# Performance work log

Measured on AMD Instinct MI355X. Metric: run time of the kernel, lower is better.

The kernel has to match this reference:

```python
import jax, jax.numpy as jnp
import numpy as np
import math

B, NH, SQ, HD = 4, 32, 512, 128
MLEN = 3584


def setup_inputs() -> dict:
    key = jax.random.key(0)
    k1, k2, k3, k4 = jax.random.split(key, 4)
    q = jax.random.normal(k1, (B, NH, SQ, HD), dtype=jnp.float32)
    k = jax.random.normal(k2, (B, NH, SQ, HD), dtype=jnp.float32)
    v = jax.random.normal(k3, (B, NH, SQ, HD), dtype=jnp.float32)
    mem = jax.random.normal(k4, (B, MLEN, 2 * NH * HD), dtype=jnp.float32)
    mask = jnp.ones((B, 1, SQ, MLEN + SQ), dtype=jnp.float32)
    return {"q": q, "k": k, "v": v, "mask": mask, "mem": mem}


def reference(q, k, v, mask, mem):
    b, nh, sq, hd = k.shape
    mlen = mem.shape[1]
    # cache_kv: stack (k,v) -> (2,b,nh,sq,hd), permute -> (b,sq,2,nh,hd), flatten
    cache_kv = jnp.stack((k, v)).transpose(1, 3, 0, 2, 4).reshape(b, sq, 2 * nh * hd)
    # split cached mem into memk/memv: (b,mlen,2,nh,hd) -> (2,b,nh,mlen,hd)
    mem_r = mem.reshape(b, mlen, 2, nh, hd).transpose(2, 0, 3, 1, 4)
    k_full = jnp.concatenate([mem_r[0], k], axis=2)  # [b,nh,mlen+sq,hd]
    v_full = jnp.concatenate([mem_r[1], v], axis=2)
    scale = 1.0 / math.sqrt(hd)
    scores = jnp.einsum("bhqd,bhkd->bhqk", q * scale, k_full)
    # standard_attention general mask path (mask.shape[-2] != 1)
    scores = scores * mask - 10000.0 * (1.0 - mask)
    probs = jax.nn.softmax(scores, axis=-1)
    context = jnp.einsum("bhqk,bhkd->bhqd", probs, v_full)
    return context, cache_kv
```

## Files before the change

kernel.cpp:

```cpp
#include <hip/hip_runtime.h>

#define B_ 4
#define NH_ 32
#define SQ_ 512
#define HD_ 128
#define MLEN_ 3584
#define KT_ 4096
#define QB_ 128
#define KB_ 64
#define NTILE_ 64
#define MEMTILES_ 56

typedef float f32x4 __attribute__((ext_vector_type(4)));
typedef short s16x8 __attribute__((ext_vector_type(8)));

__device__ __forceinline__ f32x4 MFMA16(s16x8 a, s16x8 b, f32x4 c) {
    return __builtin_amdgcn_mfma_f32_16x16x32_bf16(a, b, c, 0, 0, 0);
}

__device__ __forceinline__ s16x8 cvt8(float4 a, float4 b) {
    union { s16x8 v; __bf16 h[8]; } u;
    u.h[0] = (__bf16)a.x; u.h[1] = (__bf16)a.y;
    u.h[2] = (__bf16)a.z; u.h[3] = (__bf16)a.w;
    u.h[4] = (__bf16)b.x; u.h[5] = (__bf16)b.y;
    u.h[6] = (__bf16)b.z; u.h[7] = (__bf16)b.w;
    return u.v;
}

__launch_bounds__(512, 4)
__global__ void attn_kernel(const float* __restrict__ q, const float* __restrict__ k,
                            const float* __restrict__ v, const float* __restrict__ mask,
                            const float* __restrict__ mem, float* __restrict__ ctx)
{
    __shared__ __bf16 Klds[KB_ * HD_];
    __shared__ __bf16 Vt[HD_ * KB_];
    __shared__ __bf16 Plds[8 * 16 * KB_];

    const int tid  = threadIdx.x;
    const int lane = tid & 63;
    const int w    = tid >> 6;
    const int l15  = lane & 15;
    const int l4   = lane >> 4;
    const int xv   = (lane & 7) << 4;

    const int qt   = blockIdx.x >> 7;
    const int pair = blockIdx.x & 127;
    const int b    = pair >> 5;
    const int h    = pair & 31;
    const int q0   = qt * QB_;

    const float scale = 0.088388347648318447f;
    s16x8 qf[4];
    {
        const float* qbase = q + (((size_t)(b * NH_ + h)) * SQ_ + q0 + w * 16 + l15) * HD_;
        #pragma unroll
        for (int kc = 0; kc < 4; ++kc) {
            const float* p = qbase + kc * 32 + l4 * 8;
            float4 a = *(const float4*)p;
            float4 c = *(const float4*)(p + 4);
            a.x *= scale; a.y *= scale; a.z *= scale; a.w *= scale;
            c.x *= scale; c.y *= scale; c.z *= scale; c.w *= scale;
            qf[kc] = cvt8(a, c);
        }
    }

    f32x4 acc[8];
    #pragma unroll
    for (int n = 0; n < 8; ++n) acc[n] = (f32x4){0.f, 0.f, 0.f, 0.f};

    float mrun[4], lrun[4];
    #pragma unroll
    for (int i = 0; i < 4; ++i) { mrun[i] = -3.0e38f; lrun[i] = 0.f; }

    const float* maskbase = mask + ((size_t)b * SQ_ + q0 + w * 16 + l4 * 4) * KT_;

    for (int t = 0; t < NTILE_; ++t) {
        const int kv0 = t * KB_;
        const float *srcK, *srcV;
        int rstride;
        if (t < MEMTILES_) {
            const float* mrow = mem + ((size_t)b * MLEN_ + kv0) * (2 * NH_ * HD_) + h * HD_;
            srcK = mrow;
            srcV = mrow + NH_ * HD_;
            rstride = 2 * NH_ * HD_;
        } else {
            size_t off = (((size_t)b * NH_ + h) * SQ_ + (kv0 - MLEN_)) * HD_;
            srcK = k + off;
            srcV = v + off;
            rstride = HD_;
        }

        __syncthreads();

        #pragma unroll
        for (int it = 0; it < 2; ++it) {
            int idx = tid + it * 512;
            int row = idx >> 4, cg = idx & 15;
            const float* p = srcK + (size_t)row * rstride + cg * 8;
            float4 a = *(const float4*)p;
            float4 c = *(const float4*)(p + 4);
            s16x8 vv = cvt8(a, c);
            int byte = row * 256 + ((cg * 16) ^ ((row & 7) << 4));
            *(s16x8*)((char*)Klds + byte) = vv;
        }
        #pragma unroll
        for (int it = 0; it < 2; ++it) {
            int idx = tid + it * 512;
            int hd = idx & 127, kvb = idx >> 7;
            const float* p = srcV + (size_t)(kvb * 8) * rstride + hd;
            union { s16x8 v; __bf16 hh[8]; } u;
            #pragma unroll
            for (int j = 0; j < 8; ++j) u.hh[j] = (__bf16)p[(size_t)j * rstride];
            int byte = hd * 128 + ((kvb * 16) ^ ((hd & 7) << 4));
            *(s16x8*)((char*)Vt + byte) = u.v;
        }

        float mpre[4][4];
        #pragma unroll
        for (int i = 0; i < 4; ++i) {
            const float* mp = maskbase + (size_t)i * KT_ + kv0 + l15;
            #pragma unroll
            for (int n = 0; n < 4; ++n) mpre[i][n] = mp[n * 16];
        }

        __syncthreads();

        f32x4 sa[4];
        #pragma unroll
        for (int n = 0; n < 4; ++n) sa[n] = (f32x4){0.f, 0.f, 0.f, 0.f};
        #pragma unroll
        for (int n = 0; n < 4; ++n) {
            #pragma unroll
            for (int kc = 0; kc < 4; ++kc) {
                s16x8 kf = *(const s16x8*)((const char*)Klds +
                            (n * 16 + l15) * 256 + (((kc * 4 + l4) * 16) ^ xv));
                sa[n] = MFMA16(qf[kc], kf, sa[n]);
            }
        }

        #pragma unroll
        for (int i = 0; i < 4; ++i) {
            sa[0][i] = fmaf(mpre[i][0], sa[0][i] + 10000.f, -10000.f);
            sa[1][i] = fmaf(mpre[i][1], sa[1][i] + 10000.f, -10000.f);
            sa[2][i] = fmaf(mpre[i][2], sa[2][i] + 10000.f, -10000.f);
            sa[3][i] = fmaf(mpre[i][3], sa[3][i] + 10000.f, -10000.f);

            float rm = fmaxf(fmaxf(sa[0][i], sa[1][i]), fmaxf(sa[2][i], sa[3][i]));
            rm = fmaxf(rm, __shfl_xor(rm, 1));
            rm = fmaxf(rm, __shfl_xor(rm, 2));
            rm = fmaxf(rm, __shfl_xor(rm, 4));
            rm = fmaxf(rm, __shfl_xor(rm, 8));

            float om = mrun[i];
            float nm = fmaxf(om, rm);
            float al = __expf(om - nm);
            mrun[i] = nm;

            float rs = 0.f;
            #pragma unroll
            for (int n = 0; n < 4; ++n) {
                float pe = __expf(sa[n][i] - nm);
                sa[n][i] = pe;
                rs += pe;
            }
            rs += __shfl_xor(rs, 1);
            rs += __shfl_xor(rs, 2);
            rs += __shfl_xor(rs, 4);
            rs += __shfl_xor(rs, 8);
            lrun[i] = lrun[i] * al + rs;

            #pragma unroll
            for (int nn = 0; nn < 8; ++nn) acc[nn][i] *= al;
        }

        __bf16* pw = &Plds[w * (16 * KB_)];
        #pragma unroll
        for (int n = 0; n < 4; ++n)
            #pragma unroll
            for (int i = 0; i < 4; ++i) {
                int row = l4 * 4 + i;
                int col = n * 16 + l15;
                int byte = row * 128 + ((col * 2) ^ ((row & 7) << 4));
                *(__bf16*)((char*)pw + byte) = (__bf16)sa[n][i];
            }

        s16x8 pf[2];
        #pragma unroll
        for (int kt = 0; kt < 2; ++kt)
            pf[kt] = *(const s16x8*)((const char*)pw +
                          l15 * 128 + ((kt * 64 + l4 * 16) ^ xv));
        #pragma unroll
        for (int nn = 0; nn < 8; ++nn) {
            s16x8 vf0 = *(const s16x8*)((const char*)Vt +
                          (nn * 16 + l15) * 128 + ((l4 * 16) ^ xv));
            s16x8 vf1 = *(const s16x8*)((const char*)Vt +
                          (nn * 16 + l15) * 128 + ((64 + l4 * 16) ^ xv));
            acc[nn] = MFMA16(pf[0], vf0, acc[nn]);
            acc[nn] = MFMA16(pf[1], vf1, acc[nn]);
        }
    }

    float* obase = ctx + (((size_t)(b * NH_ + h)) * SQ_ + q0 + w * 16 + l4 * 4) * HD_ + l15;
    #pragma unroll
    for (int i = 0; i < 4; ++i) {
        float inv = 1.f / lrun[i];
        #pragma unroll
        for (int nn = 0; nn < 8; ++nn)
            obase[(size_t)i * HD_ + nn * 16] = acc[nn][i] * inv;
    }
}

__global__ void cachekv_kernel(const float* __restrict__ k, const float* __restrict__ v,
                               float* __restrict__ out)
{
    size_t i = ((size_t)blockIdx.x * 256 + threadIdx.x) * 4;
    unsigned f = (unsigned)i;
    unsigned d    = f & 127;
    unsigned hh   = (f >> 7) & 31;
    unsigned part = (f >> 12) & 1;
    unsigned s    = (f >> 13) & 511;
    unsigned bb   = f >> 22;
    const float* src = (part ? v : k) + (((size_t)(bb * 32u + hh)) * 512u + s) * 128u + d;
    *(float4*)(out + i) = *(const float4*)src;
}

extern "C" void kernel_launch(void* const* d_in, const int* in_sizes, int n_in,
                              void* d_out, int out_size, void* d_ws, size_t ws_size,
                              hipStream_t stream) {
    const float* q    = (const float*)d_in[0];
    const float* k    = (const float*)d_in[1];
    const float* v    = (const float*)d_in[2];
    const float* mask = (const float*)d_in[3];
    const float* mem  = (const float*)d_in[4];
    float* out = (float*)d_out;

    attn_kernel<<<dim3(B_ * NH_ * (SQ_ / QB_)), dim3(512), 0, stream>>>(q, k, v, mask, mem, out);

    const int ctx_elems = B_ * NH_ * SQ_ * HD_;
    const int ckv_elems = B_ * SQ_ * 2 * NH_ * HD_;
    cachekv_kernel<<<dim3(ckv_elems / 4 / 256), dim3(256), 0, stream>>>(k, v, out + ctx_elems);
    (void)in_sizes; (void)n_in; (void)out_size; (void)d_ws; (void)ws_size;
}
```

Before: 346.3 us.

## Compute transposed scores so P stays in registers, skip rescale when max stable

Swaps the MFMA operand order so each lane holds the scores for a single query row. The row max and row sum then need only two cross-lane shuffles, and the mask is read with vector loads. The shared-memory round trip for P is replaced by register shuffles that rebuild the bf16 A-operand layout. A lazy rescale skips the accumulator rescaling when the new row max stays within a threshold of the running max. This trades LDS traffic for extra shuffle instructions and a data-dependent branch.

```diff
diff --git a/kernel.cpp b/kernel.cpp
--- a/kernel.cpp
+++ b/kernel.cpp
@@ -34,7 +34,6 @@
 {
     __shared__ __bf16 Klds[KB_ * HD_];
     __shared__ __bf16 Vt[HD_ * KB_];
-    __shared__ __bf16 Plds[8 * 16 * KB_];
 
     const int tid  = threadIdx.x;
     const int lane = tid & 63;
@@ -68,11 +67,9 @@
     #pragma unroll
     for (int n = 0; n < 8; ++n) acc[n] = (f32x4){0.f, 0.f, 0.f, 0.f};
 
-    float mrun[4], lrun[4];
-    #pragma unroll
-    for (int i = 0; i < 4; ++i) { mrun[i] = -3.0e38f; lrun[i] = 0.f; }
-
-    const float* maskbase = mask + ((size_t)b * SQ_ + q0 + w * 16 + l4 * 4) * KT_;
+    float mrun = -3.0e38f, lrun = 0.f;
+
+    const float* maskrow = mask + ((size_t)b * SQ_ + q0 + w * 16 + l15) * KT_;
 
     for (int t = 0; t < NTILE_; ++t) {
         const int kv0 = t * KB_;
@@ -115,98 +112,125 @@
             *(s16x8*)((char*)Vt + byte) = u.v;
         }
 
-        float mpre[4][4];
-        #pragma unroll
-        for (int i = 0; i < 4; ++i) {
-            const float* mp = maskbase + (size_t)i * KT_ + kv0 + l15;
-            #pragma unroll
-            for (int n = 0; n < 4; ++n) mpre[i][n] = mp[n * 16];
-        }
-
         __syncthreads();
 
-        f32x4 sa[4];
-        #pragma unroll
-        for (int n = 0; n < 4; ++n) sa[n] = (f32x4){0.f, 0.f, 0.f, 0.f};
-        #pragma unroll
-        for (int n = 0; n < 4; ++n) {
+        f32x4 mk[4];
+        #pragma unroll
+        for (int mt = 0; mt < 4; ++mt)
+            mk[mt] = *(const f32x4*)(maskrow + kv0 + mt * 16 + l4 * 4);
+
+        f32x4 st[4];
+        #pragma unroll
+        for (int mt = 0; mt < 4; ++mt) st[mt] = (f32x4){0.f, 0.f, 0.f, 0.f};
+        #pragma unroll
+        for (int mt = 0; mt < 4; ++mt) {
             #pragma unroll
             for (int kc = 0; kc < 4; ++kc) {
                 s16x8 kf = *(const s16x8*)((const char*)Klds +
-                            (n * 16 + l15) * 256 + (((kc * 4 + l4) * 16) ^ xv));
-                sa[n] = MFMA16(qf[kc], kf, sa[n]);
+                            (mt * 16 + l15) * 256 + (((kc * 4 + l4) * 16) ^ xv));
+                st[mt] = MFMA16(kf, qf[kc], st[mt]);
             }
         }
 
         #pragma unroll
-        for (int i = 0; i < 4; ++i) {
-            sa[0][i] = fmaf(mpre[i][0], sa[0][i] + 10000.f, -10000.f);
-            sa[1][i] = fmaf(mpre[i][1], sa[1][i] + 10000.f, -10000.f);
-            sa[2][i] = fmaf(mpre[i][2], sa[2][i] + 10000.f, -10000.f);
-            sa[3][i] = fmaf(mpre[i][3], sa[3][i] + 10000.f, -10000.f);
-
-            float rm = fmaxf(fmaxf(sa[0][i], sa[1][i]), fmaxf(sa[2][i], sa[3][i]));
-            rm = fmaxf(rm, __shfl_xor(rm, 1));
-            rm = fmaxf(rm, __shfl_xor(rm, 2));
-            rm = fmaxf(rm, __shfl_xor(rm, 4));
-            rm = fmaxf(rm, __shfl_xor(rm, 8));
-
-            float om = mrun[i];
-            float nm = fmaxf(om, rm);
-            float al = __expf(om - nm);
-            mrun[i] = nm;
-
-            float rs = 0.f;
-            #pragma unroll
-            for (int n = 0; n < 4; ++n) {
-                float pe = __expf(sa[n][i] - nm);
-                sa[n][i] = pe;
+        for (int mt = 0; mt < 4; ++mt)
+            #pragma unroll
+            for (int r = 0; r < 4; ++r)
+                st[mt][r] = fmaf(mk[mt][r], st[mt][r] + 10000.f, -10000.f);
+
+        float x0 = fmaxf(fmaxf(st[0][0], st[0][1]), fmaxf(st[0][2], st[0][3]));
+        float x1 = fmaxf(fmaxf(st[1][0], st[1][1]), fmaxf(st[1][2], st[1][3]));
+        float x2 = fmaxf(fmaxf(st[2][0], st[2][1]), fmaxf(st[2][2], st[2][3]));
+        float x3 = fmaxf(fmaxf(st[3][0], st[3][1]), fmaxf(st[3][2], st[3][3]));
+        float rm = fmaxf(fmaxf(x0, x1), fmaxf(x2, x3));
+        rm = fmaxf(rm, __shfl_xor(rm, 16));
+        rm = fmaxf(rm, __shfl_xor(rm, 32));
+
+        if (!__all(rm <= mrun + 8.f)) {
+            float nm = fmaxf(mrun, rm);
+            float al = __expf(mrun - nm);
+            mrun = nm;
+            lrun *= al;
+            float alr0 = __shfl(al, l4 * 4 + 0);
+            float alr1 = __shfl(al, l4 * 4 + 1);
+            float alr2 = __shfl(al, l4 * 4 + 2);
+            float alr3 = __shfl(al, l4 * 4 + 3);
+            #pragma unroll
+            for (int nn = 0; nn < 8; ++nn) {
+                acc[nn][0] *= alr0; acc[nn][1] *= alr1;
+                acc[nn][2] *= alr2; acc[nn][3] *= alr3;
+            }
+        }
+
+        float rs = 0.f;
+        #pragma unroll
+        for (int mt = 0; mt < 4; ++mt) {
+            #pragma unroll
+            for (int r = 0; r < 4; ++r) {
+                float pe = __expf(st[mt][r] - mrun);
+                st[mt][r] = pe;
                 rs += pe;
             }
-            rs += __shfl_xor(rs, 1);
-            rs += __shfl_xor(rs, 2);
-            rs += __shfl_xor(rs, 4);
-            rs += __shfl_xor(rs, 8);
-            lrun[i] = lrun[i] * al + rs;
-
-            #pragma unroll
-            for (int nn = 0; nn < 8; ++nn) acc[nn][i] *= al;
-        }
-
-        __bf16* pw = &Plds[w * (16 * KB_)];
-        #pragma unroll
-        for (int n = 0; n < 4; ++n)
-            #pragma unroll
-            for (int i = 0; i < 4; ++i) {
-                int row = l4 * 4 + i;
-                int col = n * 16 + l15;
-                int byte = row * 128 + ((col * 2) ^ ((row & 7) << 4));
-                *(__bf16*)((char*)pw + byte) = (__bf16)sa[n][i];
-            }
-
-        s16x8 pf[2];
-        #pragma unroll
-        for (int kt = 0; kt < 2; ++kt)
-            pf[kt] = *(const s16x8*)((const char*)pw +
-                          l15 * 128 + ((kt * 64 + l4 * 16) ^ xv));
+        }
+        rs += __shfl_xor(rs, 16);
+        rs += __shfl_xor(rs, 32);
+        lrun += rs;
+
+        union PK { int d[2]; __bf16 hh[4]; };
+        PK pk0, pk1, pk2, pk3;
+        pk0.hh[0]=(__bf16)st[0][0]; pk0.hh[1]=(__bf16)st[0][1]; pk0.hh[2]=(__bf16)st[0][2]; pk0.hh[3]=(__bf16)st[0][3];
+        pk1.hh[0]=(__bf16)st[1][0]; pk1.hh[1]=(__bf16)st[1][1]; pk1.hh[2]=(__bf16)st[1][2]; pk1.hh[3]=(__bf16)st[1][3];
+        pk2.hh[0]=(__bf16)st[2][0]; pk2.hh[1]=(__bf16)st[2][1]; pk2.hh[2]=(__bf16)st[2][2]; pk2.hh[3]=(__bf16)st[2][3];
+        pk3.hh[0]=(__bf16)st[3][0]; pk3.hh[1]=(__bf16)st[3][1]; pk3.hh[2]=(__bf16)st[3][2]; pk3.hh[3]=(__bf16)st[3][3];
+
+        const int srcA = (l4 & 1) * 32 + l15;
+        const int srcB = srcA + 16;
+        const int sel  = l4 >> 1;
+        s16x8 pa[2];
+        {
+            union { int d[4]; s16x8 v; } ua;
+            int a00 = __shfl(pk0.d[0], srcA), a10 = __shfl(pk1.d[0], srcA);
+            int a01 = __shfl(pk0.d[1], srcA), a11 = __shfl(pk1.d[1], srcA);
+            int b00 = __shfl(pk0.d[0], srcB), b10 = __shfl(pk1.d[0], srcB);
+            int b01 = __shfl(pk0.d[1], srcB), b11 = __shfl(pk1.d[1], srcB);
+            ua.d[0] = sel ? a10 : a00; ua.d[1] = sel ? a11 : a01;
+            ua.d[2] = sel ? b10 : b00; ua.d[3] = sel ? b11 : b01;
+            pa[0] = ua.v;
+        }
+        {
+            union { int d[4]; s16x8 v; } ua;
+            int a00 = __shfl(pk2.d[0], srcA), a10 = __shfl(pk3.d[0], srcA);
+            int a01 = __shfl(pk2.d[1], srcA), a11 = __shfl(pk3.d[1], srcA);
+            int b00 = __shfl(pk2.d[0], srcB), b10 = __shfl(pk3.d[0], srcB);
+            int b01 = __shfl(pk2.d[1], srcB), b11 = __shfl(pk3.d[1], srcB);
+            ua.d[0] = sel ? a10 : a00; ua.d[1] = sel ? a11 : a01;
+            ua.d[2] = sel ? b10 : b00; ua.d[3] = sel ? b11 : b01;
+            pa[1] = ua.v;
+        }
+
         #pragma unroll
         for (int nn = 0; nn < 8; ++nn) {
             s16x8 vf0 = *(const s16x8*)((const char*)Vt +
                           (nn * 16 + l15) * 128 + ((l4 * 16) ^ xv));
             s16x8 vf1 = *(const s16x8*)((const char*)Vt +
                           (nn * 16 + l15) * 128 + ((64 + l4 * 16) ^ xv));
-            acc[nn] = MFMA16(pf[0], vf0, acc[nn]);
-            acc[nn] = MFMA16(pf[1], vf1, acc[nn]);
+            acc[nn] = MFMA16(pa[0], vf0, acc[nn]);
+            acc[nn] = MFMA16(pa[1], vf1, acc[nn]);
         }
     }
 
+    float lr0 = __shfl(lrun, l4 * 4 + 0);
+    float lr1 = __shfl(lrun, l4 * 4 + 1);
+    float lr2 = __shfl(lrun, l4 * 4 + 2);
+    float lr3 = __shfl(lrun, l4 * 4 + 3);
+    float inv0 = 1.f / lr0, inv1 = 1.f / lr1, inv2 = 1.f / lr2, inv3 = 1.f / lr3;
     float* obase = ctx + (((size_t)(b * NH_ + h)) * SQ_ + q0 + w * 16 + l4 * 4) * HD_ + l15;
     #pragma unroll
-    for (int i = 0; i < 4; ++i) {
-        float inv = 1.f / lrun[i];
-        #pragma unroll
-        for (int nn = 0; nn < 8; ++nn)
-            obase[(size_t)i * HD_ + nn * 16] = acc[nn][i] * inv;
+    for (int nn = 0; nn < 8; ++nn) {
+        obase[(size_t)0 * HD_ + nn * 16] = acc[nn][0] * inv0;
+        obase[(size_t)1 * HD_ + nn * 16] = acc[nn][1] * inv1;
+        obase[(size_t)2 * HD_ + nn * 16] = acc[nn][2] * inv2;
+        obase[(size_t)3 * HD_ + nn * 16] = acc[nn][3] * inv3;
     }
 }
 
```

Result: faster. 322.1 us (-7.0%).
